# Optimization experiments

Hardware: AMD Instinct MI355X
Metric: run time of the kernel (lower is better)

## Reference

```python
import jax, jax.numpy as jnp
import numpy as np

LOG1000 = 6.9077542789816375  # ln(1000)


def setup_inputs() -> dict:
    key = jax.random.key(0)
    kx, kp = jax.random.split(key)
    x = jax.random.normal(kx, (65536, 128), dtype=jnp.float32)
    points = jax.random.normal(kp, (2048, 128), dtype=jnp.float32)
    beta_raw = jnp.array([-3.5], dtype=jnp.float32)
    return {"x": x, "points": points, "beta_raw": beta_raw}


def reference(x, points, beta_raw):
    t1 = jnp.sum(x * x, axis=-1, keepdims=True)            # [N, 1]
    t2 = jnp.sum(points * points, axis=-1)[None, :]        # [1, P]
    t3 = 2.0 * jnp.einsum('nd,pd->np', x, points)          # [N, P]
    d2 = jnp.clip(t1 + t2 - t3, 0.0)
    min_d = jnp.min(d2, axis=-1)                           # [N]
    # translated sigmoid
    beta = jax.nn.softplus(beta_raw)                       # [1]
    alpha = -beta * LOG1000
    return jax.nn.sigmoid((min_d + alpha) / beta)
```

## Files before the change

### kernel.cpp

```cpp
#include <hip/hip_runtime.h>


#define NROWS 65536
#define NPTS  2048
#define DIMS  128
#define LOG1000F 6.9077542789816375f

typedef __attribute__((ext_vector_type(8))) int i32x8;
typedef __attribute__((ext_vector_type(4))) float f32x4;

union AFrag { int d[8]; i32x8 v; };
union BFrag { uint4 u4[2]; i32x8 v; };

__global__ __launch_bounds__(256) void prep_points_kernel(
    const float* __restrict__ pts, unsigned char* __restrict__ ptsf8,
    float* __restrict__ pnorm)
{
    int tid  = threadIdx.x;
    int lane = tid & 63;
    int w    = tid >> 6;
    int pt   = blockIdx.x * 4 + w;
    const float2 v = *reinterpret_cast<const float2*>(
        pts + (size_t)pt * DIMS + lane * 2);
    int pk = __builtin_amdgcn_cvt_pk_fp8_f32(v.x, v.y, 0, false);
    int T  = pt >> 4, pm = pt & 15;
    int q  = lane >> 4;
    int c  = (lane >> 3) & 1;
    int j  = (lane & 7) * 2;
    size_t dst = (size_t)((T * 2 + c) * 64 + q * 16 + pm) * 16 + j;
    *reinterpret_cast<unsigned short*>(ptsf8 + dst) =
        (unsigned short)(pk & 0xFFFF);
    float ss = v.x * v.x + v.y * v.y;
    ss += __shfl_xor(ss, 1, 64);
    ss += __shfl_xor(ss, 2, 64);
    ss += __shfl_xor(ss, 4, 64);
    ss += __shfl_xor(ss, 8, 64);
    ss += __shfl_xor(ss, 16, 64);
    ss += __shfl_xor(ss, 32, 64);
    if (lane == 0) pnorm[pt] = ss;
}

__global__ __launch_bounds__(256, 2) void distnet_main_kernel(
    const float* __restrict__ x, const unsigned char* __restrict__ ptsf8,
    const float* __restrict__ pnorm, const float* __restrict__ beta_raw,
    float* __restrict__ out)
{
    __shared__ __align__(16) float s_pn[NPTS];
    __shared__ float s_red[2][128];
    __shared__ float s_xn[128];

    int tid = threadIdx.x;
    {
        const float4* p4 = reinterpret_cast<const float4*>(pnorm);
        float4* d4 = reinterpret_cast<float4*>(s_pn);
        float4 a = p4[tid], b = p4[tid + 256];
        d4[tid]       = make_float4(-.5f*a.x, -.5f*a.y, -.5f*a.z, -.5f*a.w);
        d4[tid + 256] = make_float4(-.5f*b.x, -.5f*b.y, -.5f*b.z, -.5f*b.w);
    }

    int wid   = tid >> 6, lane = tid & 63;
    int m     = lane & 15, q = lane >> 4;
    int pairw = wid >> 1, half = wid & 1;
    int rbase = blockIdx.x * 128 + pairw * 64;

    AFrag afrag[4];
#pragma unroll
    for (int t = 0; t < 4; ++t) {
        const float* xp = x + (size_t)(rbase + t * 16 + m) * DIMS + q * 32;
        float s = 0.f;
#pragma unroll
        for (int d = 0; d < 8; ++d) {
            float4 v = *reinterpret_cast<const float4*>(xp + d * 4);
            int w0 = __builtin_amdgcn_cvt_pk_fp8_f32(v.x, v.y, 0, false);
            w0 = __builtin_amdgcn_cvt_pk_fp8_f32(v.z, v.w, w0, true);
            afrag[t].d[d] = w0;
            s += v.x * v.x + v.y * v.y + v.z * v.z + v.w * v.w;
        }
        s += __shfl_xor(s, 16, 64);
        s += __shfl_xor(s, 32, 64);
        if (half == 0 && q == 0) s_xn[pairw * 64 + t * 16 + m] = s;
    }
    __syncthreads();

    float runmax[4][4];
#pragma unroll
    for (int t = 0; t < 4; ++t)
#pragma unroll
        for (int r = 0; r < 4; ++r) runmax[t][r] = -1e30f;

    const uint4* bsw = reinterpret_cast<const uint4*>(ptsf8);
    const int T0 = half * 64;

    BFrag bA, bB, bC, bD;
    float pnA, pnB, pnC, pnD;

#define LOADT(gT, buf, pnh) do {                       \
        buf.u4[0] = bsw[(gT) * 128 + lane];            \
        buf.u4[1] = bsw[(gT) * 128 + 64 + lane];       \
        pnh = s_pn[(gT) * 16 + m];                     \
    } while (0)

    auto compute = [&](const BFrag& buf, float pnh) {
#pragma unroll
        for (int t = 0; t < 4; ++t) {
            f32x4 acc = {pnh, pnh, pnh, pnh};
            acc = __builtin_amdgcn_mfma_scale_f32_16x16x128_f8f6f4(
                afrag[t].v, buf.v, acc, 0, 0, 0, 0x7F7F7F7F, 0, 0x7F7F7F7F);
#pragma unroll
            for (int r = 0; r < 4; ++r)
                runmax[t][r] = fmaxf(runmax[t][r], acc[r]);
        }
    };

    LOADT(T0 + 0, bA, pnA);
    LOADT(T0 + 1, bB, pnB);
    LOADT(T0 + 2, bC, pnC);
    LOADT(T0 + 3, bD, pnD);
#pragma unroll 1
    for (int T = 0; T < 60; T += 4) {
        compute(bA, pnA);
        LOADT(T0 + T + 4, bA, pnA);
        compute(bB, pnB);
        LOADT(T0 + T + 5, bB, pnB);
        compute(bC, pnC);
        LOADT(T0 + T + 6, bC, pnC);
        compute(bD, pnD);
        LOADT(T0 + T + 7, bD, pnD);
    }
    compute(bA, pnA);
    compute(bB, pnB);
    compute(bC, pnC);
    compute(bD, pnD);
#undef LOADT

#pragma unroll
    for (int t = 0; t < 4; ++t) {
#pragma unroll
        for (int r = 0; r < 4; ++r) {
            float v = runmax[t][r];
            v = fmaxf(v, __shfl_xor(v, 1, 64));
            v = fmaxf(v, __shfl_xor(v, 2, 64));
            v = fmaxf(v, __shfl_xor(v, 4, 64));
            v = fmaxf(v, __shfl_xor(v, 8, 64));
            if (m == 0)
                s_red[half][pairw * 64 + t * 16 + q * 4 + r] = v;
        }
    }
    __syncthreads();

    if (tid < 128) {
        float vmax  = fmaxf(s_red[0][tid], s_red[1][tid]);
        float d2    = fmaxf(fmaf(-2.f, vmax, s_xn[tid]), 0.f);
        float br    = beta_raw[0];
        float beta  = log1pf(expf(br));
        float alpha = -beta * LOG1000F;
        float z     = (d2 + alpha) / beta;
        out[(size_t)blockIdx.x * 128 + tid] = 1.f / (1.f + expf(-z));
    }
}

extern "C" void kernel_launch(void* const* d_in, const int* in_sizes, int n_in,
                              void* d_out, int out_size, void* d_ws, size_t ws_size,
                              hipStream_t stream) {
    const float* x        = (const float*)d_in[0];
    const float* pts      = (const float*)d_in[1];
    const float* beta_raw = (const float*)d_in[2];
    float* out            = (float*)d_out;

    unsigned char* ptsf8 = (unsigned char*)d_ws;
    float* pnorm = (float*)((char*)d_ws + (size_t)NPTS * DIMS);

    prep_points_kernel<<<NPTS / 4, 256, 0, stream>>>(pts, ptsf8, pnorm);
    distnet_main_kernel<<<NROWS / 128, 256, 0, stream>>>(x, ptsf8, pnorm,
                                                         beta_raw, out);
    distnet_main_kernel<<<NROWS / 128, 256, 0, stream>>>(x, ptsf8, pnorm,
                                                         beta_raw, out);
}
```

Measured before the change: 114.5 us.

## Split point set across block pairs and add combine kernel, dropping duplicate launch

The main kernel now launches twice as many blocks. Each block pair covers the same 128 rows but handles half of the points, and writes a partial min-distance to workspace. A new elementwise combine kernel takes the min of the two partials, clamps it and applies the translated sigmoid. The redundant second launch of the main kernel is removed. The split is meant to raise parallelism and cut per-block loop length, at the cost of reading and converting x twice and an extra small launch with a round-trip through global memory.

Result: faster. 104.5 us (-8.8%).

```diff
diff --git a/kernel.cpp b/kernel.cpp
--- a/kernel.cpp
+++ b/kernel.cpp
@@ -42,26 +42,27 @@
 
 __global__ __launch_bounds__(256, 2) void distnet_main_kernel(
     const float* __restrict__ x, const unsigned char* __restrict__ ptsf8,
-    const float* __restrict__ pnorm, const float* __restrict__ beta_raw,
-    float* __restrict__ out)
+    const float* __restrict__ pnorm, float* __restrict__ partial)
 {
-    __shared__ __align__(16) float s_pn[NPTS];
+    __shared__ __align__(16) float s_pn[NPTS / 2];
     __shared__ float s_red[2][128];
     __shared__ float s_xn[128];
 
     int tid = threadIdx.x;
+    int g   = blockIdx.x >> 1;
+    int h   = blockIdx.x & 1;
+
     {
-        const float4* p4 = reinterpret_cast<const float4*>(pnorm);
-        float4* d4 = reinterpret_cast<float4*>(s_pn);
-        float4 a = p4[tid], b = p4[tid + 256];
-        d4[tid]       = make_float4(-.5f*a.x, -.5f*a.y, -.5f*a.z, -.5f*a.w);
-        d4[tid + 256] = make_float4(-.5f*b.x, -.5f*b.y, -.5f*b.z, -.5f*b.w);
+        const float4* p4 = reinterpret_cast<const float4*>(pnorm + h * 1024);
+        float4 a = p4[tid];
+        reinterpret_cast<float4*>(s_pn)[tid] =
+            make_float4(-.5f*a.x, -.5f*a.y, -.5f*a.z, -.5f*a.w);
     }
 
     int wid   = tid >> 6, lane = tid & 63;
     int m     = lane & 15, q = lane >> 4;
-    int pairw = wid >> 1, half = wid & 1;
-    int rbase = blockIdx.x * 128 + pairw * 64;
+    int pairw = wid >> 1, halfw = wid & 1;
+    int rbase = g * 128 + pairw * 64;
 
     AFrag afrag[4];
 #pragma unroll
@@ -78,7 +79,7 @@
         }
         s += __shfl_xor(s, 16, 64);
         s += __shfl_xor(s, 32, 64);
-        if (half == 0 && q == 0) s_xn[pairw * 64 + t * 16 + m] = s;
+        if (halfw == 0 && q == 0) s_xn[pairw * 64 + t * 16 + m] = s;
     }
     __syncthreads();
 
@@ -88,8 +89,9 @@
 #pragma unroll
         for (int r = 0; r < 4; ++r) runmax[t][r] = -1e30f;
 
-    const uint4* bsw = reinterpret_cast<const uint4*>(ptsf8);
-    const int T0 = half * 64;
+    const uint4* bsw = reinterpret_cast<const uint4*>(ptsf8)
+                       + (size_t)h * 64 * 128;
+    const int T0 = halfw * 32;
 
     BFrag bA, bB, bC, bD;
     float pnA, pnB, pnC, pnD;
@@ -117,7 +119,7 @@
     LOADT(T0 + 2, bC, pnC);
     LOADT(T0 + 3, bD, pnD);
 #pragma unroll 1
-    for (int T = 0; T < 60; T += 4) {
+    for (int T = 0; T < 28; T += 4) {
         compute(bA, pnA);
         LOADT(T0 + T + 4, bA, pnA);
         compute(bB, pnB);
@@ -143,20 +145,34 @@
             v = fmaxf(v, __shfl_xor(v, 4, 64));
             v = fmaxf(v, __shfl_xor(v, 8, 64));
             if (m == 0)
-                s_red[half][pairw * 64 + t * 16 + q * 4 + r] = v;
+                s_red[halfw][pairw * 64 + t * 16 + q * 4 + r] = v;
         }
     }
     __syncthreads();
 
     if (tid < 128) {
-        float vmax  = fmaxf(s_red[0][tid], s_red[1][tid]);
-        float d2    = fmaxf(fmaf(-2.f, vmax, s_xn[tid]), 0.f);
-        float br    = beta_raw[0];
-        float beta  = log1pf(expf(br));
-        float alpha = -beta * LOG1000F;
-        float z     = (d2 + alpha) / beta;
-        out[(size_t)blockIdx.x * 128 + tid] = 1.f / (1.f + expf(-z));
+        float vmax = fmaxf(s_red[0][tid], s_red[1][tid]);
+        partial[(size_t)h * NROWS + g * 128 + tid] =
+            fmaf(-2.f, vmax, s_xn[tid]);
     }
+}
+
+__global__ __launch_bounds__(256) void distnet_combine_kernel(
+    const float* __restrict__ partial, const float* __restrict__ beta_raw,
+    float* __restrict__ out)
+{
+    int i = blockIdx.x * 256 + threadIdx.x;
+    float4 p0 = reinterpret_cast<const float4*>(partial)[i];
+    float4 p1 = reinterpret_cast<const float4*>(partial + NROWS)[i];
+    float br    = beta_raw[0];
+    float beta  = log1pf(expf(br));
+    float alpha = -beta * LOG1000F;
+    float4 o;
+    o.x = 1.f / (1.f + expf(-(fmaxf(fminf(p0.x, p1.x), 0.f) + alpha) / beta));
+    o.y = 1.f / (1.f + expf(-(fmaxf(fminf(p0.y, p1.y), 0.f) + alpha) / beta));
+    o.z = 1.f / (1.f + expf(-(fmaxf(fminf(p0.z, p1.z), 0.f) + alpha) / beta));
+    o.w = 1.f / (1.f + expf(-(fmaxf(fminf(p0.w, p1.w), 0.f) + alpha) / beta));
+    reinterpret_cast<float4*>(out)[i] = o;
 }
 
 extern "C" void kernel_launch(void* const* d_in, const int* in_sizes, int n_in,
@@ -169,10 +185,12 @@
 
     unsigned char* ptsf8 = (unsigned char*)d_ws;
     float* pnorm = (float*)((char*)d_ws + (size_t)NPTS * DIMS);
+    float* partial = (float*)((char*)d_ws + (size_t)NPTS * DIMS
+                              + NPTS * sizeof(float));
 
     prep_points_kernel<<<NPTS / 4, 256, 0, stream>>>(pts, ptsf8, pnorm);
-    distnet_main_kernel<<<NROWS / 128, 256, 0, stream>>>(x, ptsf8, pnorm,
-                                                         beta_raw, out);
-    distnet_main_kernel<<<NROWS / 128, 256, 0, stream>>>(x, ptsf8, pnorm,
-                                                         beta_raw, out);
+    distnet_main_kernel<<<NROWS / 64, 256, 0, stream>>>(x, ptsf8, pnorm,
+                                                        partial);
+    distnet_combine_kernel<<<NROWS / 1024, 256, 0, stream>>>(partial,
+                                                             beta_raw, out);
 }
```
